# Performance work log

Measured on AMD Instinct MI355X. Metric: run time of the kernel, lower is better.

Reference implementation:

```python
import jax, jax.numpy as jnp
import numpy as np


def setup_inputs() -> dict:
    key = jax.random.key(0)
    k1, k2, k3 = jax.random.split(key, 3)
    B, C, Q, D = 64, 512, 64, 512
    H = jax.random.normal(k1, (B, C, D), dtype=jnp.float32)
    U = jax.random.normal(k2, (B, Q, D), dtype=jnp.float32)
    w = jax.random.normal(k3, (3 * D, 1), dtype=jnp.float32) * 0.02
    return {"H": H, "U": U, "w": w}


def reference(H, U, w):
    # Original: S[b,c,q] = concat([H[b,c], U[b,q], H[b,c]*U[b,q]]) @ w
    # Algebraically: split w = [w_h; w_u; w_hu] (each [D]) ->
    #   S = (H @ w_h)[:, :, None] + (U @ w_u)[:, None, :] + (H * w_hu) @ U^T
    D = H.shape[-1]
    w = w[:, 0]
    w_h, w_u, w_hu = w[:D], w[D:2 * D], w[2 * D:]
    s_h = jnp.einsum('bcd,d->bc', H, w_h)          # [B, C]
    s_u = jnp.einsum('bqd,d->bq', U, w_u)          # [B, Q]
    s_hu = jnp.einsum('bcd,bqd->bcq', H * w_hu, U)  # [B, C, Q]
    return s_h[:, :, None] + s_u[:, None, :] + s_hu
```

## Files before the change

kernel.cpp:

```cpp
#include <hip/hip_runtime.h>
#include <hip/hip_bf16.h>


#define Bn 64
#define Cn 512
#define Qn 64
#define Dn 512
#define NKT 16

typedef __bf16 bf16x8 __attribute__((ext_vector_type(8)));
typedef float  f32x4  __attribute__((ext_vector_type(4)));

__global__ __launch_bounds__(256, 2)
void sim_kernel(const float* __restrict__ H, const float* __restrict__ U,
                const float* __restrict__ w, float* __restrict__ out)
{
    __shared__ __bf16 Us[NKT][4][Qn][8];
    __shared__ float  su_l[Qn];

    const int r     = (int)blockIdx.x;
    const int b     = (r & 7) * 8 + ((r >> 3) & 7);
    const int chunk = r >> 6;
    const int c0    = chunk * 64;

    const int t    = (int)threadIdx.x;
    const int lane = t & 63;
    const int wv   = t >> 6;

    {
        const int q   = t >> 2;
        const int seg = t & 3;
        const float* __restrict__ Uq = U + ((size_t)(b * Qn + q)) * Dn;
        float su = 0.f;
#pragma unroll
        for (int j = 0; j < 16; ++j) {
            const int cc = seg + 4 * j;
            const int d0 = 8 * cc;
            f32x4 u0  = *(const f32x4*)(Uq + d0);
            f32x4 u1  = *(const f32x4*)(Uq + d0 + 4);
            f32x4 wh0 = *(const f32x4*)(w + d0);
            f32x4 wh1 = *(const f32x4*)(w + d0 + 4);
            f32x4 wu0 = *(const f32x4*)(w + 512 + d0);
            f32x4 wu1 = *(const f32x4*)(w + 512 + d0 + 4);
            f32x4 wm0 = *(const f32x4*)(w + 1024 + d0);
            f32x4 wm1 = *(const f32x4*)(w + 1024 + d0 + 4);
            bf16x8 v;
#pragma unroll
            for (int i = 0; i < 4; ++i) {
                su += wu0[i] * u0[i];
                su += wu1[i] * u1[i];
                v[i]     = (__bf16)__builtin_fmaf(wm0[i], u0[i], wh0[i]);
                v[i + 4] = (__bf16)__builtin_fmaf(wm1[i], u1[i], wh1[i]);
            }
            *(bf16x8*)&Us[cc >> 2][cc & 3][q][0] = v;
        }
        su += __shfl_xor(su, 1);
        su += __shfl_xor(su, 2);
        if (seg == 0) su_l[q] = su;
    }

    const int ql = lane & 15;
    const int hh = lane >> 4;
    const float* __restrict__ hp =
        H + ((size_t)(b * Cn + c0 + wv * 16 + ql)) * Dn + hh * 8;

    f32x4 pa[4], pb[4];
#pragma unroll
    for (int p = 0; p < 3; ++p) {
        pa[p] = *(const f32x4*)(hp + 32 * p);
        pb[p] = *(const f32x4*)(hp + 32 * p + 4);
    }

    __syncthreads();

    f32x4 acc[4] = {{0.f,0.f,0.f,0.f},{0.f,0.f,0.f,0.f},
                    {0.f,0.f,0.f,0.f},{0.f,0.f,0.f,0.f}};

#pragma unroll
    for (int k = 0; k < NKT; ++k) {
        f32x4 ca = pa[k & 3], cb = pb[k & 3];
        if (k + 3 < NKT) {
            pa[(k + 3) & 3] = *(const f32x4*)(hp + 32 * (k + 3));
            pb[(k + 3) & 3] = *(const f32x4*)(hp + 32 * (k + 3) + 4);
        }
        bf16x8 a;
#pragma unroll
        for (int i = 0; i < 4; ++i) {
            a[i]     = (__bf16)ca[i];
            a[i + 4] = (__bf16)cb[i];
        }
        bf16x8 f0 = *(const bf16x8*)&Us[k][hh][ 0 + ql][0];
        bf16x8 f1 = *(const bf16x8*)&Us[k][hh][16 + ql][0];
        bf16x8 f2 = *(const bf16x8*)&Us[k][hh][32 + ql][0];
        bf16x8 f3 = *(const bf16x8*)&Us[k][hh][48 + ql][0];
        acc[0] = __builtin_amdgcn_mfma_f32_16x16x32_bf16(a, f0, acc[0], 0, 0, 0);
        acc[1] = __builtin_amdgcn_mfma_f32_16x16x32_bf16(a, f1, acc[1], 0, 0, 0);
        acc[2] = __builtin_amdgcn_mfma_f32_16x16x32_bf16(a, f2, acc[2], 0, 0, 0);
        acc[3] = __builtin_amdgcn_mfma_f32_16x16x32_bf16(a, f3, acc[3], 0, 0, 0);
    }

    float* __restrict__ outb = out + ((size_t)(b * Cn + c0 + wv * 16)) * Qn;
#pragma unroll
    for (int fn = 0; fn < 4; ++fn) {
        const int q = fn * 16 + ql;
        const float s = su_l[q];
#pragma unroll
        for (int rr = 0; rr < 4; ++rr) {
            outb[(size_t)(hh * 4 + rr) * Qn + q] = acc[fn][rr] + s;
        }
    }
}

extern "C" void kernel_launch(void* const* d_in, const int* in_sizes, int n_in,
                              void* d_out, int out_size, void* d_ws, size_t ws_size,
                              hipStream_t stream) {
    const float* H = (const float*)d_in[0];
    const float* U = (const float*)d_in[1];
    const float* w = (const float*)d_in[2];
    float* out = (float*)d_out;
    sim_kernel<<<dim3(Bn * (Cn / 64)), dim3(256), 0, stream>>>(H, U, w, out);
}
```

Baseline: 23.77 us.

## Split U preprocessing into separate kernel and stream bf16 U fragments from global

Moves the per-batch U*w_hu+w_h bf16 conversion and the U·w_u reduction into a prep kernel that writes a fragment-ordered bf16 buffer and su values to workspace. The GEMM kernel becomes single-wave blocks (2048 blocks of 64 threads), each covering 16 rows of C. These blocks read U fragments directly from global/L2 with register prefetch instead of staging them in LDS, and no longer need a barrier. This stops each block from redundantly recomputing the U transform, at the cost of a second launch, a workspace round-trip, and more global loads per wave.

```diff
diff --git a/kernel.cpp b/kernel.cpp
--- a/kernel.cpp
+++ b/kernel.cpp
@@ -6,108 +6,113 @@
 #define Cn 512
 #define Qn 64
 #define Dn 512
-#define NKT 16
+#define WS_SU_OFF (4u * 1024u * 1024u)
 
 typedef __bf16 bf16x8 __attribute__((ext_vector_type(8)));
 typedef float  f32x4  __attribute__((ext_vector_type(4)));
 
-__global__ __launch_bounds__(256, 2)
-void sim_kernel(const float* __restrict__ H, const float* __restrict__ U,
-                const float* __restrict__ w, float* __restrict__ out)
+__global__ __launch_bounds__(256)
+void prep_kernel(const float* __restrict__ U, const float* __restrict__ w,
+                 __bf16* __restrict__ wu_out, float* __restrict__ su_out)
 {
-    __shared__ __bf16 Us[NKT][4][Qn][8];
-    __shared__ float  su_l[Qn];
+    const int bid = (int)blockIdx.x;
+    const int b   = bid >> 2;
+    const int qg  = bid & 3;
+    const int t   = (int)threadIdx.x;
+    const int q   = qg * 16 + (t >> 4);
+    const int seg = t & 15;
 
-    const int r     = (int)blockIdx.x;
-    const int b     = (r & 7) * 8 + ((r >> 3) & 7);
-    const int chunk = r >> 6;
-    const int c0    = chunk * 64;
+    const float* __restrict__ Uq = U + ((size_t)(b * Qn + q)) * Dn;
+    __bf16* __restrict__ wb = wu_out + (size_t)b * 32768;
 
-    const int t    = (int)threadIdx.x;
-    const int lane = t & 63;
-    const int wv   = t >> 6;
+    float su = 0.f;
+#pragma unroll
+    for (int j = 0; j < 4; ++j) {
+        const int d0 = seg * 32 + j * 8;
+        f32x4 u0  = *(const f32x4*)(Uq + d0);
+        f32x4 u1  = *(const f32x4*)(Uq + d0 + 4);
+        f32x4 wh0 = *(const f32x4*)(w + d0);
+        f32x4 wh1 = *(const f32x4*)(w + d0 + 4);
+        f32x4 wu0 = *(const f32x4*)(w + 512 + d0);
+        f32x4 wu1 = *(const f32x4*)(w + 512 + d0 + 4);
+        f32x4 wm0 = *(const f32x4*)(w + 1024 + d0);
+        f32x4 wm1 = *(const f32x4*)(w + 1024 + d0 + 4);
+        bf16x8 v;
+#pragma unroll
+        for (int i = 0; i < 4; ++i) {
+            su += wu0[i] * u0[i] + wu1[i] * u1[i];
+            v[i]     = (__bf16)__builtin_fmaf(wm0[i], u0[i], wh0[i]);
+            v[i + 4] = (__bf16)__builtin_fmaf(wm1[i], u1[i], wh1[i]);
+        }
+        *(bf16x8*)(wb + seg * 2048 + j * 512 + q * 8) = v;
+    }
+    su += __shfl_xor(su, 1);
+    su += __shfl_xor(su, 2);
+    su += __shfl_xor(su, 4);
+    su += __shfl_xor(su, 8);
+    if (seg == 0) su_out[b * Qn + q] = su;
+}
 
-    {
-        const int q   = t >> 2;
-        const int seg = t & 3;
-        const float* __restrict__ Uq = U + ((size_t)(b * Qn + q)) * Dn;
-        float su = 0.f;
-#pragma unroll
-        for (int j = 0; j < 16; ++j) {
-            const int cc = seg + 4 * j;
-            const int d0 = 8 * cc;
-            f32x4 u0  = *(const f32x4*)(Uq + d0);
-            f32x4 u1  = *(const f32x4*)(Uq + d0 + 4);
-            f32x4 wh0 = *(const f32x4*)(w + d0);
-            f32x4 wh1 = *(const f32x4*)(w + d0 + 4);
-            f32x4 wu0 = *(const f32x4*)(w + 512 + d0);
-            f32x4 wu1 = *(const f32x4*)(w + 512 + d0 + 4);
-            f32x4 wm0 = *(const f32x4*)(w + 1024 + d0);
-            f32x4 wm1 = *(const f32x4*)(w + 1024 + d0 + 4);
-            bf16x8 v;
-#pragma unroll
-            for (int i = 0; i < 4; ++i) {
-                su += wu0[i] * u0[i];
-                su += wu1[i] * u1[i];
-                v[i]     = (__bf16)__builtin_fmaf(wm0[i], u0[i], wh0[i]);
-                v[i + 4] = (__bf16)__builtin_fmaf(wm1[i], u1[i], wh1[i]);
-            }
-            *(bf16x8*)&Us[cc >> 2][cc & 3][q][0] = v;
-        }
-        su += __shfl_xor(su, 1);
-        su += __shfl_xor(su, 2);
-        if (seg == 0) su_l[q] = su;
-    }
+__global__ __launch_bounds__(64)
+void gemm_kernel(const float* __restrict__ H, const __bf16* __restrict__ Uw,
+                 const float* __restrict__ suw, float* __restrict__ out)
+{
+    const int r  = (int)blockIdx.x;
+    const int b  = (r & 7) * 8 + ((r >> 3) & 7);
+    const int cb = r >> 6;
 
-    const int ql = lane & 15;
-    const int hh = lane >> 4;
-    const float* __restrict__ hp =
-        H + ((size_t)(b * Cn + c0 + wv * 16 + ql)) * Dn + hh * 8;
+    const int lane = (int)threadIdx.x;
+    const int ql   = lane & 15;
+    const int hh   = lane >> 4;
 
-    f32x4 pa[4], pb[4];
+    const float*  __restrict__ hp = H  + ((size_t)(b * Cn + cb * 16 + ql)) * Dn + hh * 8;
+    const __bf16* __restrict__ up = Uw + (size_t)b * 32768 + hh * 512 + ql * 8;
+
+    f32x4  ha[4], hb[4];
+    bf16x8 uf[4][4];
+
 #pragma unroll
     for (int p = 0; p < 3; ++p) {
-        pa[p] = *(const f32x4*)(hp + 32 * p);
-        pb[p] = *(const f32x4*)(hp + 32 * p + 4);
+        ha[p] = *(const f32x4*)(hp + 32 * p);
+        hb[p] = *(const f32x4*)(hp + 32 * p + 4);
+#pragma unroll
+        for (int n = 0; n < 4; ++n)
+            uf[p][n] = *(const bf16x8*)(up + p * 2048 + n * 128);
     }
-
-    __syncthreads();
 
     f32x4 acc[4] = {{0.f,0.f,0.f,0.f},{0.f,0.f,0.f,0.f},
                     {0.f,0.f,0.f,0.f},{0.f,0.f,0.f,0.f}};
 
 #pragma unroll
-    for (int k = 0; k < NKT; ++k) {
-        f32x4 ca = pa[k & 3], cb = pb[k & 3];
-        if (k + 3 < NKT) {
-            pa[(k + 3) & 3] = *(const f32x4*)(hp + 32 * (k + 3));
-            pb[(k + 3) & 3] = *(const f32x4*)(hp + 32 * (k + 3) + 4);
+    for (int k = 0; k < 16; ++k) {
+        if (k + 3 < 16) {
+            ha[(k + 3) & 3] = *(const f32x4*)(hp + 32 * (k + 3));
+            hb[(k + 3) & 3] = *(const f32x4*)(hp + 32 * (k + 3) + 4);
+#pragma unroll
+            for (int n = 0; n < 4; ++n)
+                uf[(k + 3) & 3][n] = *(const bf16x8*)(up + (k + 3) * 2048 + n * 128);
         }
+        f32x4 ca = ha[k & 3], cb2 = hb[k & 3];
         bf16x8 a;
 #pragma unroll
         for (int i = 0; i < 4; ++i) {
             a[i]     = (__bf16)ca[i];
-            a[i + 4] = (__bf16)cb[i];
+            a[i + 4] = (__bf16)cb2[i];
         }
-        bf16x8 f0 = *(const bf16x8*)&Us[k][hh][ 0 + ql][0];
-        bf16x8 f1 = *(const bf16x8*)&Us[k][hh][16 + ql][0];
-        bf16x8 f2 = *(const bf16x8*)&Us[k][hh][32 + ql][0];
-        bf16x8 f3 = *(const bf16x8*)&Us[k][hh][48 + ql][0];
-        acc[0] = __builtin_amdgcn_mfma_f32_16x16x32_bf16(a, f0, acc[0], 0, 0, 0);
-        acc[1] = __builtin_amdgcn_mfma_f32_16x16x32_bf16(a, f1, acc[1], 0, 0, 0);
-        acc[2] = __builtin_amdgcn_mfma_f32_16x16x32_bf16(a, f2, acc[2], 0, 0, 0);
-        acc[3] = __builtin_amdgcn_mfma_f32_16x16x32_bf16(a, f3, acc[3], 0, 0, 0);
+#pragma unroll
+        for (int n = 0; n < 4; ++n)
+            acc[n] = __builtin_amdgcn_mfma_f32_16x16x32_bf16(a, uf[k & 3][n], acc[n], 0, 0, 0);
     }
 
-    float* __restrict__ outb = out + ((size_t)(b * Cn + c0 + wv * 16)) * Qn;
+    const float* __restrict__ sup  = suw + b * Qn;
+    float*       __restrict__ outb = out + ((size_t)(b * Cn + cb * 16)) * Qn;
 #pragma unroll
-    for (int fn = 0; fn < 4; ++fn) {
-        const int q = fn * 16 + ql;
-        const float s = su_l[q];
+    for (int n = 0; n < 4; ++n) {
+        const int q = n * 16 + ql;
+        const float s = sup[q];
 #pragma unroll
-        for (int rr = 0; rr < 4; ++rr) {
-            outb[(size_t)(hh * 4 + rr) * Qn + q] = acc[fn][rr] + s;
-        }
+        for (int rr = 0; rr < 4; ++rr)
+            outb[(size_t)(hh * 4 + rr) * Qn + q] = acc[n][rr] + s;
     }
 }
 
@@ -118,5 +123,10 @@
     const float* U = (const float*)d_in[1];
     const float* w = (const float*)d_in[2];
     float* out = (float*)d_out;
-    sim_kernel<<<dim3(Bn * (Cn / 64)), dim3(256), 0, stream>>>(H, U, w, out);
+
+    __bf16* ws_u  = (__bf16*)d_ws;
+    float*  ws_su = (float*)((char*)d_ws + WS_SU_OFF);
+
+    prep_kernel<<<dim3(256), dim3(256), 0, stream>>>(U, w, ws_u, ws_su);
+    gemm_kernel<<<dim3(2048), dim3(64), 0, stream>>>(H, ws_u, ws_su, out);
 }
```

After: 25.30 us. +6.5%, slower.

## Use 128-row blocks of 512 threads with swizzled U tile and earlier H prefetch

Applied to the files above, without the earlier changes.

Each block now covers 128 C rows with 8 waves, so the grid is 256 blocks instead of 512 and every U-derived bf16 tile in LDS is built once per 128 rows rather than per 64 rows. The U-preprocessing thread mapping changes so each thread handles 4 q rows over one d-slice, reduced across 32 lanes. LDS rows are XOR-swizzled by k to cut bank conflicts. The first H prefetch is issued before the U preprocessing to overlap global latency. The trade-off is fewer, larger blocks with one block per SM, which may reduce latency hiding, and 256 blocks may not fill all CUs.

```diff
diff --git a/kernel.cpp b/kernel.cpp
--- a/kernel.cpp
+++ b/kernel.cpp
@@ -6,69 +6,81 @@
 #define Cn 512
 #define Qn 64
 #define Dn 512
-#define NKT 16
 
 typedef __bf16 bf16x8 __attribute__((ext_vector_type(8)));
 typedef float  f32x4  __attribute__((ext_vector_type(4)));
 
-__global__ __launch_bounds__(256, 2)
+__global__ __launch_bounds__(512, 1)
 void sim_kernel(const float* __restrict__ H, const float* __restrict__ U,
                 const float* __restrict__ w, float* __restrict__ out)
 {
-    __shared__ __bf16 Us[NKT][4][Qn][8];
+    __shared__ __bf16 Us[16][4][64][8];
     __shared__ float  su_l[Qn];
 
-    const int r     = (int)blockIdx.x;
-    const int b     = (r & 7) * 8 + ((r >> 3) & 7);
-    const int chunk = r >> 6;
-    const int c0    = chunk * 64;
+    const int r  = (int)blockIdx.x;
+    const int x  = r & 7;
+    const int i  = r >> 3;
+    const int b  = x * 8 + (i >> 2);
+    const int c0 = (i & 3) * 128;
 
     const int t    = (int)threadIdx.x;
+    const int wv   = t >> 6;
     const int lane = t & 63;
-    const int wv   = t >> 6;
+    const int ql   = lane & 15;
+    const int hh   = lane >> 4;
+
+    const float* __restrict__ hp =
+        H + ((size_t)(b * Cn + c0 + wv * 16 + ql)) * Dn + hh * 8;
+    f32x4 ha[4], hb[4];
+#pragma unroll
+    for (int p = 0; p < 3; ++p) {
+        ha[p] = *(const f32x4*)(hp + 32 * p);
+        hb[p] = *(const f32x4*)(hp + 32 * p + 4);
+    }
 
     {
-        const int q   = t >> 2;
-        const int seg = t & 3;
-        const float* __restrict__ Uq = U + ((size_t)(b * Qn + q)) * Dn;
-        float su = 0.f;
+        const int dk = t & 31;
+        const int qg = t >> 5;
+        const int kt = dk >> 1;
+        const int cs = kt & 7;
+        float su_p[4] = {0.f, 0.f, 0.f, 0.f};
 #pragma unroll
-        for (int j = 0; j < 16; ++j) {
-            const int cc = seg + 4 * j;
-            const int d0 = 8 * cc;
-            f32x4 u0  = *(const f32x4*)(Uq + d0);
-            f32x4 u1  = *(const f32x4*)(Uq + d0 + 4);
+        for (int half = 0; half < 2; ++half) {
+            const int d0 = dk * 16 + half * 8;
+            const int hv = (dk & 1) * 2 + half;
             f32x4 wh0 = *(const f32x4*)(w + d0);
             f32x4 wh1 = *(const f32x4*)(w + d0 + 4);
             f32x4 wu0 = *(const f32x4*)(w + 512 + d0);
             f32x4 wu1 = *(const f32x4*)(w + 512 + d0 + 4);
             f32x4 wm0 = *(const f32x4*)(w + 1024 + d0);
             f32x4 wm1 = *(const f32x4*)(w + 1024 + d0 + 4);
-            bf16x8 v;
 #pragma unroll
-            for (int i = 0; i < 4; ++i) {
-                su += wu0[i] * u0[i];
-                su += wu1[i] * u1[i];
-                v[i]     = (__bf16)__builtin_fmaf(wm0[i], u0[i], wh0[i]);
-                v[i + 4] = (__bf16)__builtin_fmaf(wm1[i], u1[i], wh1[i]);
+            for (int qi = 0; qi < 4; ++qi) {
+                const int q = qg * 4 + qi;
+                const float* __restrict__ Uq =
+                    U + ((size_t)(b * Qn + q)) * Dn + d0;
+                f32x4 u0 = *(const f32x4*)Uq;
+                f32x4 u1 = *(const f32x4*)(Uq + 4);
+                bf16x8 v;
+#pragma unroll
+                for (int e = 0; e < 4; ++e) {
+                    su_p[qi] += wu0[e] * u0[e] + wu1[e] * u1[e];
+                    v[e]     = (__bf16)__builtin_fmaf(wm0[e], u0[e], wh0[e]);
+                    v[e + 4] = (__bf16)__builtin_fmaf(wm1[e], u1[e], wh1[e]);
+                }
+                *(bf16x8*)&Us[kt][hv][q ^ cs][0] = v;
             }
-            *(bf16x8*)&Us[cc >> 2][cc & 3][q][0] = v;
         }
-        su += __shfl_xor(su, 1);
-        su += __shfl_xor(su, 2);
-        if (seg == 0) su_l[q] = su;
-    }
-
-    const int ql = lane & 15;
-    const int hh = lane >> 4;
-    const float* __restrict__ hp =
-        H + ((size_t)(b * Cn + c0 + wv * 16 + ql)) * Dn + hh * 8;
-
-    f32x4 pa[4], pb[4];
 #pragma unroll
-    for (int p = 0; p < 3; ++p) {
-        pa[p] = *(const f32x4*)(hp + 32 * p);
-        pb[p] = *(const f32x4*)(hp + 32 * p + 4);
+        for (int qi = 0; qi < 4; ++qi) {
+            float v = su_p[qi];
+            v += __shfl_xor(v, 1);
+            v += __shfl_xor(v, 2);
+            v += __shfl_xor(v, 4);
+            v += __shfl_xor(v, 8);
+            v += __shfl_xor(v, 16);
+            if (dk == 0) su_l[qg * 4 + qi] = v;
+        }
     }
 
     __syncthreads();
@@ -77,22 +89,23 @@
                     {0.f,0.f,0.f,0.f},{0.f,0.f,0.f,0.f}};
 
 #pragma unroll
-    for (int k = 0; k < NKT; ++k) {
-        f32x4 ca = pa[k & 3], cb = pb[k & 3];
-        if (k + 3 < NKT) {
-            pa[(k + 3) & 3] = *(const f32x4*)(hp + 32 * (k + 3));
-            pb[(k + 3) & 3] = *(const f32x4*)(hp + 32 * (k + 3) + 4);
+    for (int k = 0; k < 16; ++k) {
+        f32x4 ca = ha[k & 3], cb = hb[k & 3];
+        if (k + 3 < 16) {
+            ha[(k + 3) & 3] = *(const f32x4*)(hp + 32 * (k + 3));
+            hb[(k + 3) & 3] = *(const f32x4*)(hp + 32 * (k + 3) + 4);
         }
         bf16x8 a;
 #pragma unroll
-        for (int i = 0; i < 4; ++i) {
-            a[i]     = (__bf16)ca[i];
-            a[i + 4] = (__bf16)cb[i];
+        for (int e = 0; e < 4; ++e) {
+            a[e]     = (__bf16)ca[e];
+            a[e + 4] = (__bf16)cb[e];
         }
-        bf16x8 f0 = *(const bf16x8*)&Us[k][hh][ 0 + ql][0];
-        bf16x8 f1 = *(const bf16x8*)&Us[k][hh][16 + ql][0];
-        bf16x8 f2 = *(const bf16x8*)&Us[k][hh][32 + ql][0];
-        bf16x8 f3 = *(const bf16x8*)&Us[k][hh][48 + ql][0];
+        const int pq = ql ^ (k & 7);
+        bf16x8 f0 = *(const bf16x8*)&Us[k][hh][pq +  0][0];
+        bf16x8 f1 = *(const bf16x8*)&Us[k][hh][pq + 16][0];
+        bf16x8 f2 = *(const bf16x8*)&Us[k][hh][pq + 32][0];
+        bf16x8 f3 = *(const bf16x8*)&Us[k][hh][pq + 48][0];
         acc[0] = __builtin_amdgcn_mfma_f32_16x16x32_bf16(a, f0, acc[0], 0, 0, 0);
         acc[1] = __builtin_amdgcn_mfma_f32_16x16x32_bf16(a, f1, acc[1], 0, 0, 0);
         acc[2] = __builtin_amdgcn_mfma_f32_16x16x32_bf16(a, f2, acc[2], 0, 0, 0);
@@ -101,13 +114,12 @@
 
     float* __restrict__ outb = out + ((size_t)(b * Cn + c0 + wv * 16)) * Qn;
 #pragma unroll
-    for (int fn = 0; fn < 4; ++fn) {
-        const int q = fn * 16 + ql;
+    for (int n = 0; n < 4; ++n) {
+        const int q = n * 16 + ql;
         const float s = su_l[q];
 #pragma unroll
-        for (int rr = 0; rr < 4; ++rr) {
-            outb[(size_t)(hh * 4 + rr) * Qn + q] = acc[fn][rr] + s;
-        }
+        for (int rr = 0; rr < 4; ++rr)
+            outb[(size_t)(hh * 4 + rr) * Qn + q] = acc[n][rr] + s;
     }
 }
 
@@ -118,5 +130,5 @@
     const float* U = (const float*)d_in[1];
     const float* w = (const float*)d_in[2];
     float* out = (float*)d_out;
-    sim_kernel<<<dim3(Bn * (Cn / 64)), dim3(256), 0, stream>>>(H, U, w, out);
+    sim_kernel<<<dim3(256), dim3(512), 0, stream>>>(H, U, w, out);
 }
```

Result: faster. 20.91 us (-12.0%).
